# Kernel optimization log

Measured on AMD Instinct MI355X. Metric: run time of the kernel, lower is better.

Reference implementation:

```python
import jax, jax.numpy as jnp
import numpy as np

# 8 voxel corner offsets in {0,1}^3 (order matches signed offsets in the
# torch module after the *0.5+0.5 remap used inside splitting/trilinear calls)
_CORNERS = np.array([[1,1,1],[1,1,0],[1,0,1],[0,1,1],[1,0,0],[0,1,0],[0,0,1],[0,0,0]], dtype=np.float32)

K = 150000   # unique corner keys (embedding rows)
V = 100000   # voxels
N = 262144   # query samples (rays * steps)
D = 64       # quantized_embed_dim


def setup_inputs() -> dict:
    key = jax.random.key(0)
    k1, k2, k3, k4, k5 = jax.random.split(key, 5)
    values = jax.random.normal(k1, (K, D), dtype=jnp.float32)
    p = jax.random.uniform(k2, (N, 3), dtype=jnp.float32)            # local trilinear coords in [0,1]
    W_proj = jax.random.normal(k3, (D, D), dtype=jnp.float32) / np.sqrt(D)
    b_proj = jnp.zeros((D,), dtype=jnp.float32)
    feats = jax.random.randint(k4, (V, 8), 0, K, dtype=jnp.int64) if jax.config.read('jax_enable_x64') else jax.random.randint(k4, (V, 8), 0, K).astype(jnp.int32)
    sample_vidx = jax.random.randint(k5, (N,), 0, V).astype(jnp.int32)
    return {"values": values, "p": p, "W_proj": W_proj, "b_proj": b_proj,
            "feats": feats, "sample_vidx": sample_vidx}


def trilinear_interp(p, q, corner_feats):
    # p: [N,3] in [0,1]; q: [8,3] corners in {0,1}; corner_feats: [N,8,D]
    # weight per corner = prod_d (p*q + (1-p)*(1-q))  -- identical to NSVF trilinear_interp
    w = jnp.prod(p[:, None, :] * q[None] + (1.0 - p[:, None, :]) * (1.0 - q[None]), axis=-1)  # [N,8]
    return jnp.einsum('nc,ncd->nd', w, corner_feats)


def reference(values, p, W_proj, b_proj, feats, sample_vidx):
    q = jnp.asarray(_CORNERS)
    corner_idx = feats[sample_vidx]          # [N,8] irregular gather of corner keys
    corner_feats = values[corner_idx]        # [N,8,D] embedding gather
    feat = trilinear_interp(p, q, corner_feats)   # [N,D]
    out = feat @ W_proj + b_proj             # values_proj Linear(embed_dim, embed_dim)
    return out
```

## Files before the change

kernel.cpp:

```cpp
#include <hip/hip_runtime.h>

#define TPB 256

typedef __attribute__((ext_vector_type(8))) short bf16x8;
typedef __attribute__((ext_vector_type(4))) float f32x4;

__device__ __forceinline__ unsigned pack_bf16_rne(float lo, float hi) {
    union { float f; unsigned u; } a, b;
    a.f = lo; b.f = hi;
    unsigned ua = (a.u + 0x7fffu + ((a.u >> 16) & 1u)) >> 16;
    unsigned ub = (b.u + 0x7fffu + ((b.u >> 16) & 1u)) >> 16;
    return ua | (ub << 16);
}
__device__ __forceinline__ unsigned short bf16_rne1(float x) {
    union { float f; unsigned u; } a; a.f = x;
    return (unsigned short)((a.u + 0x7fffu + ((a.u >> 16) & 1u)) >> 16);
}
__device__ __forceinline__ float bf_lo(unsigned u) {
    union { unsigned i; float f; } c; c.i = u << 16; return c.f;
}
__device__ __forceinline__ float bf_hi(unsigned u) {
    union { unsigned i; float f; } c; c.i = u & 0xffff0000u; return c.f;
}

__global__ __launch_bounds__(TPB) void proj_table_mfma(
    const float* __restrict__ values,
    const float* __restrict__ W,
    unsigned* __restrict__ vp,
    int K)
{
    __shared__ unsigned short tile[64 * 64];

    const int t    = threadIdx.x;
    const int l    = t & 63;
    const int w    = t >> 6;
    const int rb   = blockIdx.x * 64;
    const int r0   = rb + 16 * w;
    const int srow = l & 15;
    const int kq   = l >> 4;

    int row = r0 + srow;
    if (row >= K) row = K - 1;

    bf16x8 af[2];
    #pragma unroll
    for (int kf = 0; kf < 2; ++kf) {
        const float4 x0 = *(const float4*)&values[(size_t)row * 64 + kf * 32 + 8 * kq];
        const float4 x1 = *(const float4*)&values[(size_t)row * 64 + kf * 32 + 8 * kq + 4];
        union { unsigned u[4]; bf16x8 v; } cv;
        cv.u[0] = pack_bf16_rne(x0.x, x0.y);
        cv.u[1] = pack_bf16_rne(x0.z, x0.w);
        cv.u[2] = pack_bf16_rne(x1.x, x1.y);
        cv.u[3] = pack_bf16_rne(x1.z, x1.w);
        af[kf] = cv.v;
    }

    #pragma unroll
    for (int ct = 0; ct < 4; ++ct) {
        const int col = ct * 16 + srow;
        f32x4 acc;
        acc[0] = 0.f; acc[1] = 0.f; acc[2] = 0.f; acc[3] = 0.f;
        #pragma unroll
        for (int kf = 0; kf < 2; ++kf) {
            const int k0 = kf * 32 + 8 * kq;
            union { unsigned u[4]; bf16x8 v; } bv;
            bv.u[0] = pack_bf16_rne(W[(k0 + 0) * 64 + col], W[(k0 + 1) * 64 + col]);
            bv.u[1] = pack_bf16_rne(W[(k0 + 2) * 64 + col], W[(k0 + 3) * 64 + col]);
            bv.u[2] = pack_bf16_rne(W[(k0 + 4) * 64 + col], W[(k0 + 5) * 64 + col]);
            bv.u[3] = pack_bf16_rne(W[(k0 + 6) * 64 + col], W[(k0 + 7) * 64 + col]);
            acc = __builtin_amdgcn_mfma_f32_16x16x32_bf16(af[kf], bv.v, acc, 0, 0, 0);
        }
        #pragma unroll
        for (int r = 0; r < 4; ++r)
            tile[(16 * w + 4 * kq + r) * 64 + col] = bf16_rne1(acc[r]);
    }
    __syncthreads();

    {
        const int lrow = t >> 2;
        const int c    = t & 3;
        const int grow = rb + lrow;
        if (grow < K) {
            const uint4* src = (const uint4*)&tile[lrow * 64 + c * 16];
            uint4* dst = (uint4*)(vp + (size_t)grow * 32 + c * 8);
            dst[0] = src[0];
            dst[1] = src[1];
        }
    }
}

__global__ __launch_bounds__(TPB) void gather_interp(
    const unsigned* __restrict__ vp,
    const float* __restrict__ p,
    const float* __restrict__ b,
    const int*   __restrict__ feats,
    const int*   __restrict__ vidx,
    float* __restrict__ out,
    int N)
{
    const int t    = threadIdx.x;
    const int l    = t & 63;
    const int w    = t >> 6;
    const int base = blockIdx.x * 64 + 16 * w;
    const int srow = l & 15;
    const int kq   = l >> 4;

    const bool valid = (base + srow) < N;
    int n = base + srow;
    if (!valid) n = N - 1;

    const int v = vidx[n];
    const int4 f0 = *(const int4*)&feats[(size_t)v * 8];
    const int4 f1 = *(const int4*)&feats[(size_t)v * 8 + 4];

    const float px = p[n * 3 + 0];
    const float py = p[n * 3 + 1];
    const float pz = p[n * 3 + 2];
    const float ox = 1.0f - px, oy = 1.0f - py, oz = 1.0f - pz;
    float wgt[8];
    wgt[0] = px * py * pz;
    wgt[1] = px * py * oz;
    wgt[2] = px * oy * pz;
    wgt[3] = ox * py * pz;
    wgt[4] = px * oy * oz;
    wgt[5] = ox * py * oz;
    wgt[6] = ox * oy * pz;
    wgt[7] = ox * oy * oz;
    const int cidx[8] = {f0.x, f0.y, f0.z, f0.w, f1.x, f1.y, f1.z, f1.w};

    uint4 q0s[8], q1s[8];
    #pragma unroll
    for (int c = 0; c < 8; ++c) {
        const unsigned* row = vp + (size_t)cidx[c] * 32;
        q0s[c] = *(const uint4*)(row + 4 * kq);
        q1s[c] = *(const uint4*)(row + 16 + 4 * kq);
    }

    float a0[8] = {0.f,0.f,0.f,0.f,0.f,0.f,0.f,0.f};
    float a1[8] = {0.f,0.f,0.f,0.f,0.f,0.f,0.f,0.f};
    #pragma unroll
    for (int c = 0; c < 8; ++c) {
        const uint4 q0 = q0s[c];
        const uint4 q1 = q1s[c];
        const float wc = wgt[c];
        a0[0] = fmaf(wc, bf_lo(q0.x), a0[0]);
        a0[1] = fmaf(wc, bf_hi(q0.x), a0[1]);
        a0[2] = fmaf(wc, bf_lo(q0.y), a0[2]);
        a0[3] = fmaf(wc, bf_hi(q0.y), a0[3]);
        a0[4] = fmaf(wc, bf_lo(q0.z), a0[4]);
        a0[5] = fmaf(wc, bf_hi(q0.z), a0[5]);
        a0[6] = fmaf(wc, bf_lo(q0.w), a0[6]);
        a0[7] = fmaf(wc, bf_hi(q0.w), a0[7]);
        a1[0] = fmaf(wc, bf_lo(q1.x), a1[0]);
        a1[1] = fmaf(wc, bf_hi(q1.x), a1[1]);
        a1[2] = fmaf(wc, bf_lo(q1.y), a1[2]);
        a1[3] = fmaf(wc, bf_hi(q1.y), a1[3]);
        a1[4] = fmaf(wc, bf_lo(q1.z), a1[4]);
        a1[5] = fmaf(wc, bf_hi(q1.z), a1[5]);
        a1[6] = fmaf(wc, bf_lo(q1.w), a1[6]);
        a1[7] = fmaf(wc, bf_hi(q1.w), a1[7]);
    }

    if (valid) {
        const float4 b00 = ((const float4*)b)[2 * kq];
        const float4 b01 = ((const float4*)b)[2 * kq + 1];
        const float4 b10 = ((const float4*)b)[8 + 2 * kq];
        const float4 b11 = ((const float4*)b)[8 + 2 * kq + 1];
        f32x4* o4 = (f32x4*)(out + (size_t)n * 64);
        f32x4 v0, v1, v2, v3;
        v0[0] = a0[0] + b00.x; v0[1] = a0[1] + b00.y;
        v0[2] = a0[2] + b00.z; v0[3] = a0[3] + b00.w;
        v1[0] = a0[4] + b01.x; v1[1] = a0[5] + b01.y;
        v1[2] = a0[6] + b01.z; v1[3] = a0[7] + b01.w;
        v2[0] = a1[0] + b10.x; v2[1] = a1[1] + b10.y;
        v2[2] = a1[2] + b10.z; v2[3] = a1[3] + b10.w;
        v3[0] = a1[4] + b11.x; v3[1] = a1[5] + b11.y;
        v3[2] = a1[6] + b11.z; v3[3] = a1[7] + b11.w;
        __builtin_nontemporal_store(v0, o4 + 2 * kq);
        __builtin_nontemporal_store(v1, o4 + 2 * kq + 1);
        __builtin_nontemporal_store(v2, o4 + 8 + 2 * kq);
        __builtin_nontemporal_store(v3, o4 + 8 + 2 * kq + 1);
    }
}

__global__ __launch_bounds__(TPB) void fused_embed_proj_fp32(
    const float* __restrict__ values, const float* __restrict__ p,
    const float* __restrict__ W, const float* __restrict__ b,
    const int* __restrict__ feats, const int* __restrict__ vidx,
    float* __restrict__ out, int N)
{
    __shared__ float featS[64][68];
    __shared__ float Wlds[64][64];

    const int t    = threadIdx.x;
    const int base = blockIdx.x * 64;
    {
        const float4* Wv = (const float4*)W;
        float4*       Wl = (float4*)&Wlds[0][0];
        #pragma unroll
        for (int i = 0; i < 4; ++i) Wl[t + i * TPB] = Wv[t + i * TPB];
    }
    const int g  = t & 15;
    const int sb = t >> 4;

    int   cidx[4][8];
    float wgt[4][8];
    #pragma unroll
    for (int i = 0; i < 4; ++i) {
        const int s = sb + 16 * i;
        int n = base + s;
        if (n >= N) n = N - 1;
        const int v = vidx[n];
        const int4 f0 = *(const int4*)&feats[(size_t)v * 8];
        const int4 f1 = *(const int4*)&feats[(size_t)v * 8 + 4];
        cidx[i][0] = f0.x; cidx[i][1] = f0.y; cidx[i][2] = f0.z; cidx[i][3] = f0.w;
        cidx[i][4] = f1.x; cidx[i][5] = f1.y; cidx[i][6] = f1.z; cidx[i][7] = f1.w;
        const float px = p[n * 3], py = p[n * 3 + 1], pz = p[n * 3 + 2];
        const float ox = 1.f - px, oy = 1.f - py, oz = 1.f - pz;
        wgt[i][0] = px * py * pz; wgt[i][1] = px * py * oz;
        wgt[i][2] = px * oy * pz; wgt[i][3] = ox * py * pz;
        wgt[i][4] = px * oy * oz; wgt[i][5] = ox * py * oz;
        wgt[i][6] = ox * oy * pz; wgt[i][7] = ox * oy * oz;
    }
    #pragma unroll
    for (int i = 0; i < 4; ++i) {
        float4 acc; acc.x = acc.y = acc.z = acc.w = 0.f;
        #pragma unroll
        for (int c = 0; c < 8; ++c) {
            const float4 val = *(const float4*)&values[(size_t)cidx[i][c] * 64 + 4 * g];
            const float w = wgt[i][c];
            acc.x = fmaf(w, val.x, acc.x); acc.y = fmaf(w, val.y, acc.y);
            acc.z = fmaf(w, val.z, acc.z); acc.w = fmaf(w, val.w, acc.w);
        }
        *(float4*)&featS[sb + 16 * i][4 * g] = acc;
    }
    __syncthreads();

    const int tx = t & 15, ty = t >> 4;
    float acc[4][4];
    {
        const float4 bb = ((const float4*)b)[tx];
        #pragma unroll
        for (int j = 0; j < 4; ++j) {
            acc[j][0] = bb.x; acc[j][1] = bb.y; acc[j][2] = bb.z; acc[j][3] = bb.w;
        }
    }
    #pragma unroll 4
    for (int d = 0; d < 64; ++d) {
        const float a0 = featS[4 * ty + 0][d];
        const float a1 = featS[4 * ty + 1][d];
        const float a2 = featS[4 * ty + 2][d];
        const float a3 = featS[4 * ty + 3][d];
        const float4 wr = *(const float4*)&Wlds[d][4 * tx];
        acc[0][0] = fmaf(a0, wr.x, acc[0][0]); acc[0][1] = fmaf(a0, wr.y, acc[0][1]);
        acc[0][2] = fmaf(a0, wr.z, acc[0][2]); acc[0][3] = fmaf(a0, wr.w, acc[0][3]);
        acc[1][0] = fmaf(a1, wr.x, acc[1][0]); acc[1][1] = fmaf(a1, wr.y, acc[1][1]);
        acc[1][2] = fmaf(a1, wr.z, acc[1][2]); acc[1][3] = fmaf(a1, wr.w, acc[1][3]);
        acc[2][0] = fmaf(a2, wr.x, acc[2][0]); acc[2][1] = fmaf(a2, wr.y, acc[2][1]);
        acc[2][2] = fmaf(a2, wr.z, acc[2][2]); acc[2][3] = fmaf(a2, wr.w, acc[2][3]);
        acc[3][0] = fmaf(a3, wr.x, acc[3][0]); acc[3][1] = fmaf(a3, wr.y, acc[3][1]);
        acc[3][2] = fmaf(a3, wr.z, acc[3][2]); acc[3][3] = fmaf(a3, wr.w, acc[3][3]);
    }
    #pragma unroll
    for (int j = 0; j < 4; ++j) {
        const int n = base + 4 * ty + j;
        if (n < N) {
            float4 o; o.x = acc[j][0]; o.y = acc[j][1]; o.z = acc[j][2]; o.w = acc[j][3];
            *(float4*)&out[(size_t)n * 64 + 4 * tx] = o;
        }
    }
}

extern "C" void kernel_launch(void* const* d_in, const int* in_sizes, int n_in,
                              void* d_out, int out_size, void* d_ws, size_t ws_size,
                              hipStream_t stream) {
    const float* values = (const float*)d_in[0];
    const float* p      = (const float*)d_in[1];
    const float* W      = (const float*)d_in[2];
    const float* b      = (const float*)d_in[3];
    const int*   feats  = (const int*)d_in[4];
    const int*   vidx   = (const int*)d_in[5];
    float* out = (float*)d_out;

    const int N  = in_sizes[5];
    const int KD = in_sizes[0];
    const int K  = KD / 64;
    const int nblocks = (N + 63) / 64;

    const size_t need = (size_t)KD * 2;
    if (ws_size >= need) {
        unsigned* vp = (unsigned*)d_ws;
        const int kblocks = (K + 63) / 64;
        proj_table_mfma<<<kblocks, TPB, 0, stream>>>(values, W, vp, K);
        gather_interp<<<nblocks, TPB, 0, stream>>>(
            vp, p, b, feats, vidx, out, N);
    } else {
        fused_embed_proj_fp32<<<nblocks, TPB, 0, stream>>>(
            values, p, W, b, feats, vidx, out, N);
    }
}
```

Baseline: 72.21 us.

## Counting-sort samples by voxel before gather and fold bias into projected table

Adds a counting sort of query samples by voxel index (zero, histogram, single-block scan, atomic scatter) so that the gather kernel processes samples grouped by voxel, improving cache locality for the feats and corner-embedding lookups. The bias add moves into the projection-table kernel, which removes the per-sample bias loads. This adds four extra launches, including a serial single-block scan over 100k counters, and the output writes become scattered. Bias is now rounded to bf16 together with the projected values.

```diff
diff --git a/kernel.cpp b/kernel.cpp
--- a/kernel.cpp
+++ b/kernel.cpp
@@ -23,9 +23,60 @@
     union { unsigned i; float f; } c; c.i = u & 0xffff0000u; return c.f;
 }
 
+
+__global__ __launch_bounds__(TPB) void zero_cnt(unsigned* __restrict__ cnt, int V) {
+    const int i = blockIdx.x * TPB + threadIdx.x;
+    if (i < V) cnt[i] = 0u;
+}
+
+__global__ __launch_bounds__(TPB) void hist_kernel(
+    const int* __restrict__ vidx, unsigned* __restrict__ cnt, int N) {
+    const int i = blockIdx.x * TPB + threadIdx.x;
+    if (i < N) atomicAdd(&cnt[vidx[i]], 1u);
+}
+
+#define SCAN_T 1024
+__global__ __launch_bounds__(SCAN_T) void scan_kernel(
+    const unsigned* __restrict__ cnt, unsigned* __restrict__ offs, int V) {
+    __shared__ unsigned part[SCAN_T];
+    const int t = threadIdx.x;
+    const int chunk = (V + SCAN_T - 1) / SCAN_T;
+    const int s = t * chunk;
+    const int e = (s + chunk < V) ? s + chunk : V;
+
+    unsigned sum = 0;
+    for (int i = s; i < e; ++i) sum += cnt[i];
+    part[t] = sum;
+    __syncthreads();
+    for (int d = 1; d < SCAN_T; d <<= 1) {
+        unsigned v = (t >= d) ? part[t - d] : 0u;
+        __syncthreads();
+        part[t] += v;
+        __syncthreads();
+    }
+    unsigned run = (t == 0) ? 0u : part[t - 1];
+    for (int i = s; i < e; ++i) {
+        offs[i] = run;
+        run += cnt[i];
+    }
+}
+
+__global__ __launch_bounds__(TPB) void scatter_kernel(
+    const int* __restrict__ vidx, unsigned* __restrict__ offs,
+    int* __restrict__ sorted, int* __restrict__ svox, int N) {
+    const int i = blockIdx.x * TPB + threadIdx.x;
+    if (i < N) {
+        const int v = vidx[i];
+        const unsigned pos = atomicAdd(&offs[v], 1u);
+        sorted[pos] = i;
+        svox[pos]   = v;
+    }
+}
+
 __global__ __launch_bounds__(TPB) void proj_table_mfma(
     const float* __restrict__ values,
     const float* __restrict__ W,
+    const float* __restrict__ b,
     unsigned* __restrict__ vp,
     int K)
 {
@@ -58,6 +109,7 @@
     #pragma unroll
     for (int ct = 0; ct < 4; ++ct) {
         const int col = ct * 16 + srow;
+        const float bias = b[col];
         f32x4 acc;
         acc[0] = 0.f; acc[1] = 0.f; acc[2] = 0.f; acc[3] = 0.f;
         #pragma unroll
@@ -72,7 +124,7 @@
         }
         #pragma unroll
         for (int r = 0; r < 4; ++r)
-            tile[(16 * w + 4 * kq + r) * 64 + col] = bf16_rne1(acc[r]);
+            tile[(16 * w + 4 * kq + r) * 64 + col] = bf16_rne1(acc[r] + bias);
     }
     __syncthreads();
 
@@ -92,9 +144,10 @@
 __global__ __launch_bounds__(TPB) void gather_interp(
     const unsigned* __restrict__ vp,
     const float* __restrict__ p,
-    const float* __restrict__ b,
     const int*   __restrict__ feats,
     const int*   __restrict__ vidx,
+    const int*   __restrict__ sorted,
+    const int*   __restrict__ svox,
     float* __restrict__ out,
     int N)
 {
@@ -105,11 +158,19 @@
     const int srow = l & 15;
     const int kq   = l >> 4;
 
-    const bool valid = (base + srow) < N;
-    int n = base + srow;
-    if (!valid) n = N - 1;
-
-    const int v = vidx[n];
+    const int  slot  = base + srow;
+    const bool valid = slot < N;
+    const int  cs    = valid ? slot : N - 1;
+
+    int n, v;
+    if (sorted) {
+        n = sorted[cs];
+        v = svox[cs];
+    } else {
+        n = cs;
+        v = vidx[n];
+    }
+
     const int4 f0 = *(const int4*)&feats[(size_t)v * 8];
     const int4 f1 = *(const int4*)&feats[(size_t)v * 8 + 4];
 
@@ -162,20 +223,12 @@
     }
 
     if (valid) {
-        const float4 b00 = ((const float4*)b)[2 * kq];
-        const float4 b01 = ((const float4*)b)[2 * kq + 1];
-        const float4 b10 = ((const float4*)b)[8 + 2 * kq];
-        const float4 b11 = ((const float4*)b)[8 + 2 * kq + 1];
         f32x4* o4 = (f32x4*)(out + (size_t)n * 64);
         f32x4 v0, v1, v2, v3;
-        v0[0] = a0[0] + b00.x; v0[1] = a0[1] + b00.y;
-        v0[2] = a0[2] + b00.z; v0[3] = a0[3] + b00.w;
-        v1[0] = a0[4] + b01.x; v1[1] = a0[5] + b01.y;
-        v1[2] = a0[6] + b01.z; v1[3] = a0[7] + b01.w;
-        v2[0] = a1[0] + b10.x; v2[1] = a1[1] + b10.y;
-        v2[2] = a1[2] + b10.z; v2[3] = a1[3] + b10.w;
-        v3[0] = a1[4] + b11.x; v3[1] = a1[5] + b11.y;
-        v3[2] = a1[6] + b11.z; v3[3] = a1[7] + b11.w;
+        v0[0] = a0[0]; v0[1] = a0[1]; v0[2] = a0[2]; v0[3] = a0[3];
+        v1[0] = a0[4]; v1[1] = a0[5]; v1[2] = a0[6]; v1[3] = a0[7];
+        v2[0] = a1[0]; v2[1] = a1[1]; v2[2] = a1[2]; v2[3] = a1[3];
+        v3[0] = a1[4]; v3[1] = a1[5]; v3[2] = a1[6]; v3[3] = a1[7];
         __builtin_nontemporal_store(v0, o4 + 2 * kq);
         __builtin_nontemporal_store(v1, o4 + 2 * kq + 1);
         __builtin_nontemporal_store(v2, o4 + 8 + 2 * kq);
@@ -285,15 +338,39 @@
     const int N  = in_sizes[5];
     const int KD = in_sizes[0];
     const int K  = KD / 64;
+    const int V  = in_sizes[4] / 8;
     const int nblocks = (N + 63) / 64;
 
-    const size_t need = (size_t)KD * 2;
-    if (ws_size >= need) {
+    auto align256 = [](size_t x) { return (x + 255) & ~(size_t)255; };
+    const size_t vp_off     = 0;
+    const size_t vp_bytes   = align256((size_t)KD * 2);
+    const size_t cnt_off    = vp_bytes;
+    const size_t cnt_bytes  = align256((size_t)V * 4);
+    const size_t offs_off   = cnt_off + cnt_bytes;
+    const size_t sorted_off = offs_off + cnt_bytes;
+    const size_t svox_off   = sorted_off + align256((size_t)N * 4);
+    const size_t need_sort  = svox_off + align256((size_t)N * 4);
+    const size_t need_vp    = (size_t)KD * 2;
+
+    if (ws_size >= need_sort) {
+        unsigned* vp     = (unsigned*)((char*)d_ws + vp_off);
+        unsigned* cnt    = (unsigned*)((char*)d_ws + cnt_off);
+        unsigned* offs   = (unsigned*)((char*)d_ws + offs_off);
+        int*      sorted = (int*)((char*)d_ws + sorted_off);
+        int*      svox   = (int*)((char*)d_ws + svox_off);
+
+        zero_cnt<<<(V + TPB - 1) / TPB, TPB, 0, stream>>>(cnt, V);
+        hist_kernel<<<(N + TPB - 1) / TPB, TPB, 0, stream>>>(vidx, cnt, N);
+        scan_kernel<<<1, SCAN_T, 0, stream>>>(cnt, offs, V);
+        scatter_kernel<<<(N + TPB - 1) / TPB, TPB, 0, stream>>>(vidx, offs, sorted, svox, N);
+        proj_table_mfma<<<(K + 63) / 64, TPB, 0, stream>>>(values, W, b, vp, K);
+        gather_interp<<<nblocks, TPB, 0, stream>>>(
+            vp, p, feats, vidx, sorted, svox, out, N);
+    } else if (ws_size >= need_vp) {
         unsigned* vp = (unsigned*)d_ws;
-        const int kblocks = (K + 63) / 64;
-        proj_table_mfma<<<kblocks, TPB, 0, stream>>>(values, W, vp, K);
+        proj_table_mfma<<<(K + 63) / 64, TPB, 0, stream>>>(values, W, b, vp, K);
         gather_interp<<<nblocks, TPB, 0, stream>>>(
-            vp, p, b, feats, vidx, out, N);
+            vp, p, feats, vidx, nullptr, nullptr, out, N);
     } else {
         fused_embed_proj_fp32<<<nblocks, TPB, 0, stream>>>(
             values, p, W, b, feats, vidx, out, N);
```

After: 245.6 us. +240.1%, slower.
